# Optimization experiments

Measured on AMD Instinct MI355X. Metric: run time of the kernel, lower is better.

## Reference

```python
import jax, jax.numpy as jnp
import numpy as np

KSIZE = 3

def setup_inputs() -> dict:
    key = jax.random.key(0)
    k1, k2, k3, k4 = jax.random.split(key, 4)
    B, C, H, W = 4, 64, 256, 512
    x = jax.random.normal(k1, (B, C, H, W), dtype=jnp.float32)
    # precomputed latitude-dependent resampling index into flattened H*W
    idx_flat = jax.random.randint(k2, (KSIZE * H * KSIZE * W,), 0, H * W, dtype=jnp.int64)
    weight = jax.random.normal(k3, (C, C, KSIZE, KSIZE), dtype=jnp.float32) * 0.05
    bias = jax.random.normal(k4, (C,), dtype=jnp.float32) * 0.05
    return {"x": x, "idx_flat": idx_flat, "weight": weight, "bias": bias}

def reference(x, idx_flat, weight, bias):
    B, C, H, W = x.shape
    k = KSIZE
    # latitude-dependent scaled gather: [B, C, H*W] -> [B, C, k*H, k*W]
    x1d = x.reshape(B, C, H * W)
    scaled = jnp.take(x1d, idx_flat, axis=2).reshape(B, C, k * H, k * W)
    # conv with kernel=stride=k, no padding -> [B, C, H, W]
    out = jax.lax.conv_general_dilated(
        scaled, weight,
        window_strides=(k, k), padding='VALID',
        dimension_numbers=('NCHW', 'OIHW', 'NCHW'))
    return out + bias[None, :, None, None]
```

## Files before the change

kernel.cpp:

```cpp
#include <hip/hip_runtime.h>
#include <stdint.h>

#define HW_   131072
#define W_    512
#define C_    64
#define KDIM  576

typedef __bf16 bf16_t;
typedef bf16_t bf16x8 __attribute__((ext_vector_type(8)));
typedef float  f32x4_t __attribute__((ext_vector_type(4)));
typedef float  f32x2_t __attribute__((ext_vector_type(2)));
typedef unsigned u32x4 __attribute__((ext_vector_type(4)));

__device__ __forceinline__ unsigned short f32_to_bf16(float f) {
    union { float f; unsigned u; } v; v.f = f;
    unsigned r = (v.u + 0x7FFFu + ((v.u >> 16) & 1u)) >> 16;
    return (unsigned short)r;
}

__device__ __forceinline__ unsigned pack_bf16(float a, float b) {
    union { unsigned u; __bf16 h[2]; } pk;
    pk.h[0] = (__bf16)a;
    pk.h[1] = (__bf16)b;
    return pk.u;
}

#define XT_BYTES   67108864ull
#define WF_BYTES   73728ull

__global__ __launch_bounds__(256) void k_prep_w(const float* __restrict__ w,
                                                unsigned short* __restrict__ wfrag) {
    int id = blockIdx.x * 256 + threadIdx.x;
    if (id >= 18 * 4 * 64) return;
    int lane = id & 63;
    int nt   = (id >> 6) & 3;
    int kc   = id >> 8;
    int n  = nt * 16 + (lane & 15);
    int k0 = kc * 32 + ((lane >> 4) << 3);
    unsigned short tmp[8];
#pragma unroll
    for (int j = 0; j < 8; ++j) {
        int k = k0 + j;
        int t = k >> 6;
        int c = k & 63;
        tmp[j] = f32_to_bf16(w[(size_t)n * KDIM + c * 9 + t]);
    }
    uint4 v;
    v.x = tmp[0] | ((unsigned)tmp[1] << 16);
    v.y = tmp[2] | ((unsigned)tmp[3] << 16);
    v.z = tmp[4] | ((unsigned)tmp[5] << 16);
    v.w = tmp[6] | ((unsigned)tmp[7] << 16);
    ((uint4*)wfrag)[id] = v;
}

__global__ __launch_bounds__(256) void k_transpose(const float* __restrict__ x,
                                                   unsigned short* __restrict__ xt) {
    __shared__ unsigned short tile[256][66];
    int t    = threadIdx.x;
    int lane = t & 63;
    int wave = t >> 6;
    int gp0 = blockIdx.x * 256;
    int b  = gp0 >> 17;
    int p0 = gp0 & (HW_ - 1);
    const float* xb = x + ((size_t)b * C_) * HW_ + p0;
#pragma unroll
    for (int it = 0; it < 16; ++it) {
        int c0  = (it & 7) * 8 + wave * 2;
        int px0 = ((it >> 3) << 7) + lane * 2;
        const float* s0 = xb + ((size_t)c0 << 17) + px0;
        f32x2_t v0 = __builtin_nontemporal_load((const f32x2_t*)s0);
        f32x2_t v1 = __builtin_nontemporal_load((const f32x2_t*)(s0 + HW_));
        *(unsigned*)&tile[px0 + 0][c0] = pack_bf16(v0.x, v1.x);
        *(unsigned*)&tile[px0 + 1][c0] = pack_bf16(v0.y, v1.y);
    }
    __syncthreads();
    unsigned short* dst = xt + (size_t)gp0 * C_;
#pragma unroll
    for (int it = 0; it < 8; ++it) {
        int cid = it * 256 + t;
        int px  = cid >> 3;
        int ch  = cid & 7;
        uint4 v;
        v.x = *(unsigned*)&tile[px][ch * 8 + 0];
        v.y = *(unsigned*)&tile[px][ch * 8 + 2];
        v.z = *(unsigned*)&tile[px][ch * 8 + 4];
        v.w = *(unsigned*)&tile[px][ch * 8 + 6];
        ((uint4*)(dst + (size_t)px * C_))[ch] = v;
    }
}

__global__ __launch_bounds__(256, 2) void k_gemm(const unsigned short* __restrict__ xt,
                                                 const unsigned short* __restrict__ wfrag,
                                                 const int* __restrict__ idx,
                                                 const float* __restrict__ bias,
                                                 float* __restrict__ out) {
    __shared__ u32x4 blds[4096];

    int tid  = threadIdx.x;
    int wave = tid >> 6;
    int lane = tid & 63;
    int bid  = blockIdx.x;
    int gbase = (((bid & 7) << 9) + (bid >> 3)) * 128;
    int b = gbase >> 17;

    int quad = lane >> 4;
    int col  = lane & 15;
    int pxw  = wave * 32;

    {
        const u32x4* wfv = (const u32x4*)wfrag;
#pragma unroll
        for (int i = 0; i < 16; ++i)
            blds[i * 256 + tid] = wfv[i * 256 + tid];
    }

    unsigned p_reg[9][2];
#pragma unroll
    for (int ms = 0; ms < 2; ++ms) {
        int g  = gbase + pxw + ms * 16 + col;
        int hw = g & (HW_ - 1);
        int h = hw >> 9, w = hw & (W_ - 1);
        const int* ib = idx + (size_t)(3 * h) * (3 * W_) + 3 * w;
#pragma unroll
        for (int t = 0; t < 9; ++t)
            p_reg[t][ms] = (unsigned)ib[(t / 3) * (3 * W_) + (t % 3)];
    }

    __syncthreads();

    const unsigned short* xtb = xt + (((size_t)b) << 17) * C_;

    f32x4_t acc[2][4] = {};
    u32x4 Abuf[8][2];
    u32x4 Bp[2][4];
    u32x4 Bt[2][4];

#define GLOADX4(dst, addr)                                                       \
    asm volatile("global_load_dwordx4 %0, %1, off"                               \
                 : "=&v"(dst) : "v"((const void*)(addr)) : "memory")
#define WAITVM(n)                                                                \
    { asm volatile("s_waitcnt vmcnt(" #n ")" ::: "memory");                      \
      __builtin_amdgcn_sched_barrier(0); }
#define ISSUE_A(s)                                                               \
    { const int t_ = (s) >> 1, h_ = (s) & 1;                                     \
      GLOADX4(Abuf[(s) & 7][0], (const char*)xtb +                               \
              (((size_t)p_reg[t_][0] << 7) + (h_ << 6) + (quad << 4)));          \
      GLOADX4(Abuf[(s) & 7][1], (const char*)xtb +                               \
              (((size_t)p_reg[t_][1] << 7) + (h_ << 6) + (quad << 4))); }
#define READ_B(s)                                                                \
    { _Pragma("unroll")                                                          \
      for (int nt = 0; nt < 4; ++nt)                                             \
          Bp[(s) & 1][nt] = blds[((s) * 4 + nt) * 64 + lane]; }
#define MFMA8(s, BSRC)                                                           \
    { _Pragma("unroll")                                                          \
      for (int ms = 0; ms < 2; ++ms)                                             \
      _Pragma("unroll")                                                          \
      for (int nt = 0; nt < 4; ++nt)                                             \
          acc[ms][nt] = __builtin_amdgcn_mfma_f32_16x16x32_bf16(                 \
              __builtin_bit_cast(bf16x8, Abuf[(s) & 7][ms]),                     \
              __builtin_bit_cast(bf16x8, (BSRC)[nt]), acc[ms][nt], 0, 0, 0); }

    {
        const char* wfb = (const char*)wfrag;
#pragma unroll
        for (int nt = 0; nt < 4; ++nt)
            GLOADX4(Bt[0][nt], wfb + (size_t)((16 * 4 + nt) * 64 + lane) * 16);
#pragma unroll
        for (int nt = 0; nt < 4; ++nt)
            GLOADX4(Bt[1][nt], wfb + (size_t)((17 * 4 + nt) * 64 + lane) * 16);
    }
    ISSUE_A(0) ISSUE_A(1) ISSUE_A(2) ISSUE_A(3)
    ISSUE_A(4) ISSUE_A(5) ISSUE_A(6) ISSUE_A(7)

    READ_B(0)

    WAITVM(14) READ_B(1)  MFMA8(0,  Bp[0]) ISSUE_A(8)
    WAITVM(14) READ_B(2)  MFMA8(1,  Bp[1]) ISSUE_A(9)
    WAITVM(14) READ_B(3)  MFMA8(2,  Bp[0]) ISSUE_A(10)
    WAITVM(14) READ_B(4)  MFMA8(3,  Bp[1]) ISSUE_A(11)
    WAITVM(14) READ_B(5)  MFMA8(4,  Bp[0]) ISSUE_A(12)
    WAITVM(14) READ_B(6)  MFMA8(5,  Bp[1]) ISSUE_A(13)
    WAITVM(14) READ_B(7)  MFMA8(6,  Bp[0]) ISSUE_A(14)
    WAITVM(14) READ_B(8)  MFMA8(7,  Bp[1]) ISSUE_A(15)
    WAITVM(14) READ_B(9)  MFMA8(8,  Bp[0]) ISSUE_A(16)
    WAITVM(14) READ_B(10) MFMA8(9,  Bp[1]) ISSUE_A(17)
    WAITVM(14) READ_B(11) MFMA8(10, Bp[0])
    WAITVM(12) READ_B(12) MFMA8(11, Bp[1])
    WAITVM(10) READ_B(13) MFMA8(12, Bp[0])
    WAITVM(8)  READ_B(14) MFMA8(13, Bp[1])
    WAITVM(6)  READ_B(15) MFMA8(14, Bp[0])
    WAITVM(4)             MFMA8(15, Bp[1])
    WAITVM(2)             MFMA8(16, Bt[0])
    WAITVM(0)             MFMA8(17, Bt[1])

#undef GLOADX4
#undef WAITVM
#undef ISSUE_A
#undef READ_B
#undef MFMA8

#pragma unroll
    for (int nt = 0; nt < 4; ++nt) {
        int o = nt * 16 + col;
        float bv = bias[o];
#pragma unroll
        for (int ms = 0; ms < 2; ++ms) {
            int m0 = ms * 16 + quad * 4;
            int hw0 = (gbase + pxw + m0) & (HW_ - 1);
            f32x4_t v = acc[ms][nt];
            v.x += bv; v.y += bv; v.z += bv; v.w += bv;
            *(f32x4_t*)(out + (((size_t)(b * 64 + o)) << 17) + hw0) = v;
        }
    }
}

__global__ __launch_bounds__(256) void k_fallback(const float* __restrict__ x,
                                                  const int* __restrict__ idx,
                                                  const float* __restrict__ w,
                                                  const float* __restrict__ bias,
                                                  float* __restrict__ out) {
    size_t g = (size_t)blockIdx.x * 256 + threadIdx.x;
    int hw = (int)(g & (HW_ - 1));
    int o  = (int)((g >> 17) & 63);
    int b  = (int)(g >> 23);
    int h = hw >> 9, ww = hw & (W_ - 1);
    size_t ibase = (size_t)(3 * h) * (3 * W_) + 3 * ww;
    int p[9];
#pragma unroll
    for (int th = 0; th < 3; ++th)
#pragma unroll
        for (int tw = 0; tw < 3; ++tw)
            p[th * 3 + tw] = idx[ibase + (size_t)th * (3 * W_) + tw];
    const float* xb = x + (size_t)b * C_ * HW_;
    const float* wo = w + (size_t)o * KDIM;
    float acc = bias[o];
    for (int c = 0; c < C_; ++c) {
        const float* xc = xb + (size_t)c * HW_;
        const float* wc = wo + c * 9;
#pragma unroll
        for (int t = 0; t < 9; ++t)
            acc += xc[p[t]] * wc[t];
    }
    out[g] = acc;
}

extern "C" void kernel_launch(void* const* d_in, const int* in_sizes, int n_in,
                              void* d_out, int out_size, void* d_ws, size_t ws_size,
                              hipStream_t stream) {
    const float* x    = (const float*)d_in[0];
    const int*   idx  = (const int*)d_in[1];
    const float* w    = (const float*)d_in[2];
    const float* bias = (const float*)d_in[3];
    float* out = (float*)d_out;

    if (ws_size >= XT_BYTES + WF_BYTES) {
        unsigned short* xt    = (unsigned short*)d_ws;
        unsigned short* wfrag = (unsigned short*)((char*)d_ws + XT_BYTES);
        k_prep_w   <<<18,   256, 0, stream>>>(w, wfrag);
        k_transpose<<<2048, 256, 0, stream>>>(x, xt);
        k_gemm     <<<4096, 256, 0, stream>>>(xt, wfrag, idx, bias, out);
    } else {
        k_fallback<<<131072, 256, 0, stream>>>(x, idx, w, bias, out);
    }
}
```

Measured before the change: 329.8 us.

## Halve LDS weight staging and stream later weight k-steps from global memory

The GEMM kernel now stages only the first 8 k-steps of weight fragments in LDS (halving shared memory per block) and streams weight fragments for k-steps 8-17 directly from global/L2 into a double-buffered register set, interleaved with the A gathers under retuned vmcnt waits. The aim is to cut LDS footprint and the upfront weight copy, possibly allowing more resident blocks. The cost is extra global load traffic and a tighter vmcnt pipeline, where memory latency can stall the MFMAs. Separately, the transpose kernel switches from nontemporal loads to ordinary loads.

```diff
diff --git a/kernel.cpp b/kernel.cpp
--- a/kernel.cpp
+++ b/kernel.cpp
@@ -68,8 +68,8 @@
         int c0  = (it & 7) * 8 + wave * 2;
         int px0 = ((it >> 3) << 7) + lane * 2;
         const float* s0 = xb + ((size_t)c0 << 17) + px0;
-        f32x2_t v0 = __builtin_nontemporal_load((const f32x2_t*)s0);
-        f32x2_t v1 = __builtin_nontemporal_load((const f32x2_t*)(s0 + HW_));
+        f32x2_t v0 = *(const f32x2_t*)s0;
+        f32x2_t v1 = *(const f32x2_t*)(s0 + HW_);
         *(unsigned*)&tile[px0 + 0][c0] = pack_bf16(v0.x, v1.x);
         *(unsigned*)&tile[px0 + 1][c0] = pack_bf16(v0.y, v1.y);
     }
@@ -94,7 +94,7 @@
                                                  const int* __restrict__ idx,
                                                  const float* __restrict__ bias,
                                                  float* __restrict__ out) {
-    __shared__ u32x4 blds[4096];
+    __shared__ u32x4 blds[2048];
 
     int tid  = threadIdx.x;
     int wave = tid >> 6;
@@ -110,7 +110,7 @@
     {
         const u32x4* wfv = (const u32x4*)wfrag;
 #pragma unroll
-        for (int i = 0; i < 16; ++i)
+        for (int i = 0; i < 8; ++i)
             blds[i * 256 + tid] = wfv[i * 256 + tid];
     }
 
@@ -129,11 +129,12 @@
     __syncthreads();
 
     const unsigned short* xtb = xt + (((size_t)b) << 17) * C_;
+    const char* wfb = (const char*)wfrag;
 
     f32x4_t acc[2][4] = {};
     u32x4 Abuf[8][2];
     u32x4 Bp[2][4];
-    u32x4 Bt[2][4];
+    u32x4 Bf[2][4];
 
 #define GLOADX4(dst, addr)                                                       \
     asm volatile("global_load_dwordx4 %0, %1, off"                               \
@@ -147,6 +148,11 @@
               (((size_t)p_reg[t_][0] << 7) + (h_ << 6) + (quad << 4)));          \
       GLOADX4(Abuf[(s) & 7][1], (const char*)xtb +                               \
               (((size_t)p_reg[t_][1] << 7) + (h_ << 6) + (quad << 4))); }
+#define ISSUE_BF(s)                                                              \
+    { _Pragma("unroll")                                                          \
+      for (int nt = 0; nt < 4; ++nt)                                             \
+          GLOADX4(Bf[(s) & 1][nt],                                               \
+                  wfb + (size_t)(((s) * 4 + nt) * 64 + lane) * 16); }
 #define READ_B(s)                                                                \
     { _Pragma("unroll")                                                          \
       for (int nt = 0; nt < 4; ++nt)                                             \
@@ -160,42 +166,34 @@
               __builtin_bit_cast(bf16x8, Abuf[(s) & 7][ms]),                     \
               __builtin_bit_cast(bf16x8, (BSRC)[nt]), acc[ms][nt], 0, 0, 0); }
 
-    {
-        const char* wfb = (const char*)wfrag;
-#pragma unroll
-        for (int nt = 0; nt < 4; ++nt)
-            GLOADX4(Bt[0][nt], wfb + (size_t)((16 * 4 + nt) * 64 + lane) * 16);
-#pragma unroll
-        for (int nt = 0; nt < 4; ++nt)
-            GLOADX4(Bt[1][nt], wfb + (size_t)((17 * 4 + nt) * 64 + lane) * 16);
-    }
     ISSUE_A(0) ISSUE_A(1) ISSUE_A(2) ISSUE_A(3)
     ISSUE_A(4) ISSUE_A(5) ISSUE_A(6) ISSUE_A(7)
 
     READ_B(0)
 
-    WAITVM(14) READ_B(1)  MFMA8(0,  Bp[0]) ISSUE_A(8)
-    WAITVM(14) READ_B(2)  MFMA8(1,  Bp[1]) ISSUE_A(9)
-    WAITVM(14) READ_B(3)  MFMA8(2,  Bp[0]) ISSUE_A(10)
-    WAITVM(14) READ_B(4)  MFMA8(3,  Bp[1]) ISSUE_A(11)
-    WAITVM(14) READ_B(5)  MFMA8(4,  Bp[0]) ISSUE_A(12)
-    WAITVM(14) READ_B(6)  MFMA8(5,  Bp[1]) ISSUE_A(13)
-    WAITVM(14) READ_B(7)  MFMA8(6,  Bp[0]) ISSUE_A(14)
-    WAITVM(14) READ_B(8)  MFMA8(7,  Bp[1]) ISSUE_A(15)
-    WAITVM(14) READ_B(9)  MFMA8(8,  Bp[0]) ISSUE_A(16)
-    WAITVM(14) READ_B(10) MFMA8(9,  Bp[1]) ISSUE_A(17)
-    WAITVM(14) READ_B(11) MFMA8(10, Bp[0])
-    WAITVM(12) READ_B(12) MFMA8(11, Bp[1])
-    WAITVM(10) READ_B(13) MFMA8(12, Bp[0])
-    WAITVM(8)  READ_B(14) MFMA8(13, Bp[1])
-    WAITVM(6)  READ_B(15) MFMA8(14, Bp[0])
-    WAITVM(4)             MFMA8(15, Bp[1])
-    WAITVM(2)             MFMA8(16, Bt[0])
-    WAITVM(0)             MFMA8(17, Bt[1])
+    WAITVM(14) READ_B(1) MFMA8(0, Bp[0])              ISSUE_A(8)
+    WAITVM(14) READ_B(2) MFMA8(1, Bp[1])              ISSUE_A(9)
+    WAITVM(14) READ_B(3) MFMA8(2, Bp[0])              ISSUE_A(10)
+    WAITVM(14) READ_B(4) MFMA8(3, Bp[1])              ISSUE_A(11)
+    WAITVM(14) READ_B(5) MFMA8(4, Bp[0])              ISSUE_A(12)
+    WAITVM(14) READ_B(6) MFMA8(5, Bp[1])              ISSUE_A(13)
+    WAITVM(14) READ_B(7) MFMA8(6, Bp[0]) ISSUE_BF(8)  ISSUE_A(14)
+    WAITVM(18)           MFMA8(7, Bp[1]) ISSUE_BF(9)  ISSUE_A(15)
+    WAITVM(8)            MFMA8(8, Bf[0]) ISSUE_BF(10) ISSUE_A(16)
+    WAITVM(8)            MFMA8(9, Bf[1]) ISSUE_BF(11) ISSUE_A(17)
+    WAITVM(8)            MFMA8(10, Bf[0]) ISSUE_BF(12)
+    WAITVM(6)            MFMA8(11, Bf[1]) ISSUE_BF(13)
+    WAITVM(4)            MFMA8(12, Bf[0]) ISSUE_BF(14)
+    WAITVM(4)            MFMA8(13, Bf[1]) ISSUE_BF(15)
+    WAITVM(4)            MFMA8(14, Bf[0]) ISSUE_BF(16)
+    WAITVM(4)            MFMA8(15, Bf[1]) ISSUE_BF(17)
+    WAITVM(4)            MFMA8(16, Bf[0])
+    WAITVM(0)            MFMA8(17, Bf[1])
 
 #undef GLOADX4
 #undef WAITVM
 #undef ISSUE_A
+#undef ISSUE_BF
 #undef READ_B
 #undef MFMA8
 
```

New measurement: 347.5 us. +5.4%, slower.
